# Kernel optimization log

Measured on AMD Instinct MI355X. Metric: run time of the kernel, lower is better.

## Reference

```python
import jax, jax.numpy as jnp
import numpy as np

N, IN_C, OUT_C, H = 100000, 256, 64, 8
K_CURV = 1.0      # manifold curvature k (Lorentz: t = sqrt(||s||^2 + k))
POWER_K = 2.0     # power_k of fp feature map


def fp(x, p):
    # norm(x) / (norm(x**p) + eps) * x**p, norms over last dim
    eps = 1e-12
    xp = x ** p
    norm_x = jnp.linalg.norm(x, axis=-1, keepdims=True)
    norm_xp = jnp.linalg.norm(xp, axis=-1, keepdims=True)
    return norm_x / (norm_xp + eps) * xp


def setup_inputs() -> dict:
    key = jax.random.key(0)
    ks = jax.random.split(key, 8)
    s = 1.0 / np.sqrt(IN_C)
    sm = 1.0 / np.sqrt(OUT_C)
    return {
        "query_input": jax.random.normal(ks[0], (N, IN_C), jnp.float32),
        # per-head HypLinear weights (stacked over heads)
        "Wq": jax.random.uniform(ks[1], (H, IN_C, OUT_C), jnp.float32, -s, s),
        "bq": jnp.zeros((H, OUT_C), jnp.float32),
        "Wk": jax.random.uniform(ks[2], (H, IN_C, OUT_C), jnp.float32, -s, s),
        "bk": jnp.zeros((H, OUT_C), jnp.float32),
        "Wv": jax.random.uniform(ks[3], (H, IN_C, OUT_C), jnp.float32, -s, s),
        "bv": jnp.zeros((H, OUT_C), jnp.float32),
        "norm_scale": jnp.ones((), jnp.float32),
        # v_map_mlp: Linear(out_channels, out_channels)
        "Wm": jax.random.uniform(ks[4], (OUT_C, OUT_C), jnp.float32, -sm, sm),
        "bm": jnp.zeros((OUT_C,), jnp.float32),
    }


def reference(query_input, Wq, bq, Wk, bk, Wv, bv, norm_scale, Wm, bm):
    # HypLinear per head: space part = x @ W + b; the time part
    # sqrt(||space||^2 + k) is dropped by [..., 1:] in linear_focus_attention,
    # so only the space components are computed.  shapes: [N, H, OUT_C]
    qs = jnp.einsum('nd,hdo->nho', query_input, Wq) + bq
    ks_ = jnp.einsum('nd,hdo->nho', query_input, Wk) + bk
    v = jnp.einsum('nd,hdo->nho', query_input, Wv) + bv

    denom_s = jnp.abs(norm_scale) + 1e-6
    phi_q = fp((jax.nn.relu(qs) + 1e-6) / denom_s, POWER_K)
    phi_k = fp((jax.nn.relu(ks_) + 1e-6) / denom_s, POWER_K)

    # linear attention: O(N * H * m * d)
    kT_v = jnp.einsum('nhm,nhd->hmd', phi_k, v)          # [H, m, d]
    numerator = jnp.einsum('nhm,hmd->nhd', phi_q, kT_v)  # [N, H, d]
    sum_k = phi_k.sum(axis=0)                            # [H, m]
    denominator = jnp.einsum('nhd,hd->nh', phi_q, sum_k)[..., None]
    attn = numerator / (denominator + 1e-6)

    # residual v-map MLP
    attn = attn + (jnp.einsum('nhd,de->nhe', v, Wm) + bm)

    # trans_heads_concat=False -> mean over heads
    out = attn.mean(axis=1)                              # [N, OUT_C]

    # lift back to Lorentz: prepend time component
    t = jnp.sqrt((out ** 2).sum(axis=-1, keepdims=True) + K_CURV)
    return jnp.concatenate([t, out], axis=-1)            # [N, OUT_C+1]
```

## Files before the change

kernel.cpp:

```cpp
#include <hip/hip_runtime.h>
#include <hip/hip_bf16.h>

#define NROWS 100000
#define NH 8
#define RPC 1568
#define NSUB 49
#define K2CH 98

typedef short s16x8 __attribute__((ext_vector_type(8)));
typedef float f32x4 __attribute__((ext_vector_type(4)));
typedef unsigned short u16;

__device__ __forceinline__ u16 f2bf(float f) {
  union { float f; unsigned u; } x; x.f = f;
  unsigned r = (x.u + 0x7FFFu + ((x.u >> 16) & 1u)) >> 16;
  return (u16)r;
}
__device__ __forceinline__ float bf2f(u16 b) {
  union { unsigned u; float f; } x; x.u = ((unsigned)b) << 16;
  return x.f;
}

__global__ __launch_bounds__(256) void k0_pack(
    const float* __restrict__ Wq, const float* __restrict__ Wk,
    const float* __restrict__ Wv, u16* __restrict__ Wp)
{
  int t = blockIdx.x * 256 + threadIdx.x;
  int lane = t & 63;
  int rest = t >> 6;
  int s = rest % 48;
  int hc = rest / 48;
  int c2 = hc & 1, h = hc >> 1;
  int ml = lane & 15, sgk = lane >> 4;
  const float* W; int col, ks;
  if (s < 32) { int tl = s >> 3; ks = s & 7; W = c2 ? Wk : Wq; col = tl * 16 + ml; }
  else        { int tv = (s >> 3) - 4; ks = s & 7; W = Wv; col = c2 * 32 + tv * 16 + ml; }
  int k0 = ks * 32 + sgk * 8;
  u16 o[8];
#pragma unroll
  for (int j = 0; j < 8; j++)
    o[j] = f2bf(W[((size_t)h * 256 + k0 + j) * 64 + col]);
  ushort4* dst = (ushort4*)(Wp + (size_t)t * 8);
  dst[0] = make_ushort4(o[0], o[1], o[2], o[3]);
  dst[1] = make_ushort4(o[4], o[5], o[6], o[7]);
}

__global__ __launch_bounds__(256, 2) void k1_gemm_phi(
    const float* __restrict__ x, const u16* __restrict__ Wp,
    const float* __restrict__ bq, const float* __restrict__ bk,
    const float* __restrict__ bv, const float* __restrict__ nsc,
    u16* __restrict__ phi_q, u16* __restrict__ phi_k, u16* __restrict__ vout)
{
  __shared__ u16 xs[32 * 256];
  __shared__ u16 vws[32 * 64 * 8];
  __shared__ u16 stq[4 * 16 * 72];
  __shared__ u16 stv[32 * 72];
  __shared__ float biasl[192];

  const int tid = threadIdx.x;
  const int wv = tid >> 6, lane = tid & 63;
  const int c2 = wv & 1, rg = wv >> 1;
  const int m = lane & 15, sg = lane >> 4;
  const int rc = blockIdx.x & 63, h = blockIdx.x >> 6;
  const int n0 = rc * RPC;

  if (tid < 192) {
    const float* bp = tid < 64 ? bq : (tid < 128 ? bk : bv);
    biasl[tid] = bp[h * 64 + (tid & 63)];
  }

  const u16* wb = Wp + (size_t)(h * 2 + c2) * (48 * 64 * 8);
  s16x8 wq[4][8];
#pragma unroll
  for (int t = 0; t < 4; t++)
#pragma unroll
    for (int ks = 0; ks < 8; ks++)
      wq[t][ks] = *(const s16x8*)(wb + ((t * 8 + ks) * 64 + lane) * 8);

#pragma unroll
  for (int i2 = 0; i2 < 8; i2++) {
    int u = tid + i2 * 256;
    int tl = u >> 9, ks = (u >> 6) & 7, ln = u & 63;
    const u16* src = Wp + ((size_t)(h * 2 + (tl >> 1)) * 48 + 32 + (tl & 1) * 8 + ks) * (64 * 8)
                     + (size_t)ln * 8;
    *(s16x8*)(vws + (size_t)u * 8) = *(const s16x8*)src;
  }

#pragma unroll
  for (int i = 0; i < 4; i++) {
    int cu = tid + i * 256;
    int row = cu >> 5, c = cu & 31;
    int n = n0 + row; if (n >= NROWS) n = NROWS - 1;
    const float* src = x + (size_t)n * 256 + c * 8;
    float4 f0 = *(const float4*)src;
    float4 f1 = *(const float4*)(src + 4);
    s16x8 pk;
    pk[0] = (short)f2bf(f0.x); pk[1] = (short)f2bf(f0.y);
    pk[2] = (short)f2bf(f0.z); pk[3] = (short)f2bf(f0.w);
    pk[4] = (short)f2bf(f1.x); pk[5] = (short)f2bf(f1.y);
    pk[6] = (short)f2bf(f1.z); pk[7] = (short)f2bf(f1.w);
    *(s16x8*)(xs + row * 256 + ((c ^ (row & 7)) * 8)) = pk;
  }
  __syncthreads();

  const float inv_denom = 1.0f / (fabsf(nsc[0]) + 1e-6f);
  u16* const xbase = xs + (rg * 16 + m) * 256;
  const int sw = m & 7;

  for (int s = 0; s < NSUB; s++) {
    float4 xl[8];
    if (s + 1 < NSUB) {
      int nb = n0 + (s + 1) * 32;
#pragma unroll
      for (int i = 0; i < 4; i++) {
        int cu = tid + i * 256;
        int row = cu >> 5, c = cu & 31;
        int n = nb + row; if (n >= NROWS) n = NROWS - 1;
        const float* src = x + (size_t)n * 256 + c * 8;
        xl[i * 2]     = *(const float4*)src;
        xl[i * 2 + 1] = *(const float4*)(src + 4);
      }
    }

    f32x4 aq[4], av[2];
#pragma unroll
    for (int t = 0; t < 4; t++) aq[t] = (f32x4){0.f, 0.f, 0.f, 0.f};
    av[0] = (f32x4){0.f, 0.f, 0.f, 0.f};
    av[1] = (f32x4){0.f, 0.f, 0.f, 0.f};
#pragma unroll
    for (int ks = 0; ks < 8; ks++) {
      s16x8 bf = *(const s16x8*)(xbase + (((ks * 4 + sg) ^ sw) * 8));
#pragma unroll
      for (int t = 0; t < 4; t++)
        aq[t] = __builtin_amdgcn_mfma_f32_16x16x32_bf16(wq[t][ks], bf, aq[t], 0, 0, 0);
      s16x8 vw0 = *(const s16x8*)(vws + (((c2 * 2 + 0) * 8 + ks) * 64 + lane) * 8);
      s16x8 vw1 = *(const s16x8*)(vws + (((c2 * 2 + 1) * 8 + ks) * 64 + lane) * 8);
      av[0] = __builtin_amdgcn_mfma_f32_16x16x32_bf16(vw0, bf, av[0], 0, 0, 0);
      av[1] = __builtin_amdgcn_mfma_f32_16x16x32_bf16(vw1, bf, av[1], 0, 0, 0);
    }

    f32x4 bqk[4], bvv[2];
#pragma unroll
    for (int t = 0; t < 4; t++) bqk[t] = *(const f32x4*)&biasl[c2 * 64 + t * 16 + sg * 4];
#pragma unroll
    for (int tv = 0; tv < 2; tv++) bvv[tv] = *(const f32x4*)&biasl[128 + c2 * 32 + tv * 16 + sg * 4];

    float vq[4][4];
    float s2 = 0.f, s4 = 0.f;
#pragma unroll
    for (int t = 0; t < 4; t++)
#pragma unroll
      for (int r = 0; r < 4; r++) {
        float y = (fmaxf(aq[t][r] + bqk[t][r], 0.f) + 1e-6f) * inv_denom;
        float y2 = y * y;
        vq[t][r] = y2;
        s2 += y2; s4 += y2 * y2;
      }
    s2 += __shfl_xor(s2, 16); s2 += __shfl_xor(s2, 32);
    s4 += __shfl_xor(s4, 16); s4 += __shfl_xor(s4, 32);
    float sc = sqrtf(s2) / (sqrtf(s4) + 1e-12f);

    {
      u16* sq = stq + wv * 1152 + m * 72;
#pragma unroll
      for (int t = 0; t < 4; t++)
        *(ushort4*)(sq + ((t + m) & 3) * 16 + sg * 4) =
          make_ushort4(f2bf(vq[t][0] * sc), f2bf(vq[t][1] * sc),
                       f2bf(vq[t][2] * sc), f2bf(vq[t][3] * sc));
      int rowl = rg * 16 + m;
      u16* sv = stv + rowl * 72;
#pragma unroll
      for (int tv = 0; tv < 2; tv++) {
        int tc = c2 * 2 + tv;
        f32x4 a = av[tv], b = bvv[tv];
        *(ushort4*)(sv + ((tc + rowl) & 3) * 16 + sg * 4) =
          make_ushort4(f2bf(a[0] + b[0]), f2bf(a[1] + b[1]),
                       f2bf(a[2] + b[2]), f2bf(a[3] + b[3]));
      }
    }
    {
      int r_ = lane >> 2, tc = lane & 3;
      const u16* a = stq + wv * 1152 + r_ * 72 + ((tc + r_) & 3) * 16;
      s16x8 p0 = *(const s16x8*)a;
      s16x8 p1 = *(const s16x8*)(a + 8);
      int n = n0 + s * 32 + rg * 16 + r_;
      if (n < NROWS) {
        u16* dst = (c2 ? phi_k : phi_q) + ((size_t)h * NROWS + n) * 64 + tc * 16;
        *(s16x8*)dst = p0;
        *(s16x8*)(dst + 8) = p1;
      }
    }
    __syncthreads();

    {
      int row = wv * 8 + (lane >> 3);
      int hc8 = lane & 7, tc = hc8 >> 1, half = hc8 & 1;
      const u16* a = stv + row * 72 + ((tc + row) & 3) * 16 + half * 8;
      s16x8 pv = *(const s16x8*)a;
      int n = n0 + s * 32 + row;
      if (n < NROWS)
        *(s16x8*)(vout + ((size_t)h * NROWS + n) * 64 + tc * 16 + half * 8) = pv;
    }
    if (s + 1 < NSUB) {
#pragma unroll
      for (int i = 0; i < 4; i++) {
        int cu = tid + i * 256;
        int row = cu >> 5, c = cu & 31;
        float4 f0 = xl[i * 2], f1 = xl[i * 2 + 1];
        s16x8 pk;
        pk[0] = (short)f2bf(f0.x); pk[1] = (short)f2bf(f0.y);
        pk[2] = (short)f2bf(f0.z); pk[3] = (short)f2bf(f0.w);
        pk[4] = (short)f2bf(f1.x); pk[5] = (short)f2bf(f1.y);
        pk[6] = (short)f2bf(f1.z); pk[7] = (short)f2bf(f1.w);
        *(s16x8*)(xs + row * 256 + ((c ^ (row & 7)) * 8)) = pk;
      }
    }
    __syncthreads();
  }
}

__global__ __launch_bounds__(256) void k2_ktv(
    const u16* __restrict__ phi_k, const u16* __restrict__ vin,
    float* __restrict__ P)
{
  __shared__ u16 pkT[2][64][72];
  __shared__ u16 vT[2][64][72];
  const int tid = threadIdx.x;
  const int h = blockIdx.y;
  const int r0 = blockIdx.x * 1024;
  const int wv = tid >> 6, lane = tid & 63;
  const int m = lane & 15, sg = lane >> 4;
  const int c4 = (tid & 15) * 4, rgp = tid >> 4;

  const u16* pkb = phi_k + (size_t)h * (NROWS * 64);
  const u16* vb  = vin  + (size_t)h * (NROWS * 64);

  f32x4 acc[4];
#pragma unroll
  for (int t = 0; t < 4; t++) acc[t] = (f32x4){0.f, 0.f, 0.f, 0.f};
  f32x4 accs = (f32x4){0.f, 0.f, 0.f, 0.f};
  s16x8 onesf;
#pragma unroll
  for (int j = 0; j < 8; j++) onesf[j] = (m == 0) ? (short)0x3F80 : (short)0;

  ushort4 pk4[4], vv4[4];
#define K2_LOAD(sub)                                                        \
  {                                                                         \
    int nb = r0 + (sub) * 64 + rgp * 4;                                     \
    _Pragma("unroll")                                                       \
    for (int i = 0; i < 4; i++) {                                           \
      int n = nb + i;                                                       \
      if (n < NROWS) {                                                      \
        pk4[i] = *(const ushort4*)(pkb + (size_t)n * 64 + c4);              \
        vv4[i] = *(const ushort4*)(vb  + (size_t)n * 64 + c4);              \
      } else {                                                              \
        pk4[i] = make_ushort4(0, 0, 0, 0);                                  \
        vv4[i] = make_ushort4(0, 0, 0, 0);                                  \
      }                                                                     \
    }                                                                       \
  }
#define K2_WRITE(buf)                                                       \
  {                                                                         \
    *(ushort4*)&pkT[buf][c4 + 0][rgp * 4] = make_ushort4(pk4[0].x, pk4[1].x, pk4[2].x, pk4[3].x); \
    *(ushort4*)&pkT[buf][c4 + 1][rgp * 4] = make_ushort4(pk4[0].y, pk4[1].y, pk4[2].y, pk4[3].y); \
    *(ushort4*)&pkT[buf][c4 + 2][rgp * 4] = make_ushort4(pk4[0].z, pk4[1].z, pk4[2].z, pk4[3].z); \
    *(ushort4*)&pkT[buf][c4 + 3][rgp * 4] = make_ushort4(pk4[0].w, pk4[1].w, pk4[2].w, pk4[3].w); \
    *(ushort4*)&vT[buf][c4 + 0][rgp * 4]  = make_ushort4(vv4[0].x, vv4[1].x, vv4[2].x, vv4[3].x); \
    *(ushort4*)&vT[buf][c4 + 1][rgp * 4]  = make_ushort4(vv4[0].y, vv4[1].y, vv4[2].y, vv4[3].y); \
    *(ushort4*)&vT[buf][c4 + 2][rgp * 4]  = make_ushort4(vv4[0].z, vv4[1].z, vv4[2].z, vv4[3].z); \
    *(ushort4*)&vT[buf][c4 + 3][rgp * 4]  = make_ushort4(vv4[0].w, vv4[1].w, vv4[2].w, vv4[3].w); \
  }

  K2_LOAD(0); K2_WRITE(0);
  __syncthreads();

  for (int sub = 0; sub < 16; sub++) {
    int cur = sub & 1;
    if (sub + 1 < 16) K2_LOAD(sub + 1);
#pragma unroll
    for (int ks = 0; ks < 2; ks++) {
      s16x8 af = *(const s16x8*)&pkT[cur][wv * 16 + m][ks * 32 + sg * 8];
#pragma unroll
      for (int t = 0; t < 4; t++) {
        s16x8 bfv = *(const s16x8*)&vT[cur][t * 16 + m][ks * 32 + sg * 8];
        acc[t] = __builtin_amdgcn_mfma_f32_16x16x32_bf16(af, bfv, acc[t], 0, 0, 0);
      }
      accs = __builtin_amdgcn_mfma_f32_16x16x32_bf16(af, onesf, accs, 0, 0, 0);
    }
    if (sub + 1 < 16) K2_WRITE(cur ^ 1);
    __syncthreads();
  }

  float* pb = P + (size_t)(blockIdx.x * NH + h) * (65 * 64);
  int mm = wv * 16 + sg * 4;
#pragma unroll
  for (int t = 0; t < 4; t++)
#pragma unroll
    for (int r = 0; r < 4; r++)
      pb[(t * 16 + m) * 64 + mm + r] = acc[t][r];
  if (m == 0)
#pragma unroll
    for (int r = 0; r < 4; r++)
      pb[64 * 64 + mm + r] = accs[r];
}

__global__ __launch_bounds__(256) void k25_pack(
    const float* __restrict__ P, const float* __restrict__ Wm,
    u16* __restrict__ kTvT, u16* __restrict__ WmP)
{
  int idx = blockIdx.x * 256 + threadIdx.x;
  if (idx < NH * 65 * 64) {
    float s = 0.f;
    for (int rcc = 0; rcc < K2CH; rcc++)
      s += P[(size_t)rcc * (NH * 65 * 64) + idx];
    kTvT[idx] = f2bf(s);
  } else if (idx < NH * 65 * 64 + 64 * 64) {
    int j = idx - NH * 65 * 64;
    WmP[j] = f2bf(Wm[(j & 63) * 64 + (j >> 6)]);
  }
}

__global__ __launch_bounds__(256) void k3_out(
    const u16* __restrict__ phi_q, const u16* __restrict__ vin,
    const u16* __restrict__ kTvT, const u16* __restrict__ WmP,
    const float* __restrict__ bm, float* __restrict__ out)
{
  const int tid = threadIdx.x;
  const int wv = tid >> 6, lane = tid & 63;
  const int m = lane & 15, sg = lane >> 4;
  const int n0 = blockIdx.x * 64;
  const int rw = wv * 16;
  const int n = n0 + rw + m;

  float bmv[4];
#pragma unroll
  for (int t = 0; t < 4; t++) bmv[t] = bm[t * 16 + m];

  s16x8 vbf[2];
#pragma unroll
  for (int ks = 0; ks < 2; ks++) {
    float a[8];
#pragma unroll
    for (int j = 0; j < 8; j++) a[j] = 0.f;
#pragma unroll
    for (int h = 0; h < NH; h++) {
      s16x8 v8 = *(const s16x8*)(vin + (size_t)h * (NROWS * 64) + (size_t)n * 64
                                 + ks * 32 + sg * 8);
#pragma unroll
      for (int j = 0; j < 8; j++) a[j] += bf2f((u16)v8[j]);
    }
#pragma unroll
    for (int j = 0; j < 8; j++) vbf[ks][j] = (short)f2bf(a[j] * 0.125f);
  }

  f32x4 zero4 = {0.f, 0.f, 0.f, 0.f};
  s16x8 zero8 = {0, 0, 0, 0, 0, 0, 0, 0};
  f32x4 osum[4];
#pragma unroll
  for (int t = 0; t < 4; t++) osum[t] = zero4;

  for (int h = 0; h < NH; h++) {
    const u16* pqb = phi_q + (size_t)h * (NROWS * 64) + (size_t)n * 64;
    const u16* kb = kTvT + (size_t)h * (65 * 64);
    f32x4 accn[4];
#pragma unroll
    for (int t = 0; t < 4; t++) accn[t] = zero4;
    f32x4 accd = zero4;
#pragma unroll
    for (int ks = 0; ks < 2; ks++) {
      s16x8 aq = *(const s16x8*)(pqb + ks * 32 + sg * 8);
#pragma unroll
      for (int t = 0; t < 4; t++) {
        s16x8 bfv = *(const s16x8*)(kb + (size_t)(t * 16 + m) * 64 + ks * 32 + sg * 8);
        accn[t] = __builtin_amdgcn_mfma_f32_16x16x32_bf16(aq, bfv, accn[t], 0, 0, 0);
      }
      s16x8 bd = zero8;
      if (m == 0)
        bd = *(const s16x8*)(kb + (size_t)64 * 64 + ks * 32 + sg * 8);
      accd = __builtin_amdgcn_mfma_f32_16x16x32_bf16(aq, bd, accd, 0, 0, 0);
    }
#pragma unroll
    for (int r = 0; r < 4; r++) {
      float den = __shfl(accd[r], lane & 48);
      float rinv = 1.0f / (den + 1e-6f);
#pragma unroll
      for (int t = 0; t < 4; t++) osum[t][r] += accn[t][r] * rinv;
    }
  }

  f32x4 accr[4];
#pragma unroll
  for (int t = 0; t < 4; t++) accr[t] = zero4;
#pragma unroll
  for (int ks = 0; ks < 2; ks++)
#pragma unroll
    for (int t = 0; t < 4; t++) {
      s16x8 bw = *(const s16x8*)(WmP + (size_t)(t * 16 + m) * 64 + ks * 32 + sg * 8);
      accr[t] = __builtin_amdgcn_mfma_f32_16x16x32_bf16(vbf[ks], bw, accr[t], 0, 0, 0);
    }

#pragma unroll
  for (int r = 0; r < 4; r++) {
    int nn = n0 + rw + sg * 4 + r;
    float v4[4];
    float ssq = 0.f;
#pragma unroll
    for (int t = 0; t < 4; t++) {
      float o = osum[t][r] * 0.125f + accr[t][r] + bmv[t];
      v4[t] = o;
      ssq += o * o;
    }
    ssq += __shfl_xor(ssq, 1);
    ssq += __shfl_xor(ssq, 2);
    ssq += __shfl_xor(ssq, 4);
    ssq += __shfl_xor(ssq, 8);
    if (nn < NROWS) {
      if (m == 0) out[(size_t)nn * 65] = sqrtf(ssq + 1.0f);
#pragma unroll
      for (int t = 0; t < 4; t++)
        out[(size_t)nn * 65 + 1 + t * 16 + m] = v4[t];
    }
  }
}

extern "C" void kernel_launch(void* const* d_in, const int* in_sizes, int n_in,
                              void* d_out, int out_size, void* d_ws, size_t ws_size,
                              hipStream_t stream) {
  const float* x   = (const float*)d_in[0];
  const float* Wq  = (const float*)d_in[1];
  const float* bq  = (const float*)d_in[2];
  const float* Wk  = (const float*)d_in[3];
  const float* bk  = (const float*)d_in[4];
  const float* Wv  = (const float*)d_in[5];
  const float* bv  = (const float*)d_in[6];
  const float* nsc = (const float*)d_in[7];
  const float* Wm  = (const float*)d_in[8];
  const float* bm  = (const float*)d_in[9];
  float* out = (float*)d_out;

  char* ws = (char*)d_ws;
  const size_t PHI_BYTES = (size_t)NROWS * NH * 64 * 2;
  u16* phi_q = (u16*)(ws);
  u16* phi_k = (u16*)(ws + PHI_BYTES);
  u16* vv    = (u16*)(ws + 2 * PHI_BYTES);
  u16* Wp    = (u16*)(ws + 3 * PHI_BYTES);
  char* p    = ws + 3 * PHI_BYTES + 786432;
  float* P   = (float*)(p);
  u16* kTvT  = (u16*)(p + 13066240);
  u16* WmP   = (u16*)(p + 13066240 + 66560);

  k0_pack<<<192, 256, 0, stream>>>(Wq, Wk, Wv, Wp);
  k1_gemm_phi<<<512, 256, 0, stream>>>(x, Wp, bq, bk, bv, nsc, phi_q, phi_k, vv);
  dim3 g2(K2CH, NH);
  k2_ktv<<<g2, 256, 0, stream>>>(phi_k, vv, P);
  k25_pack<<<(NH * 65 * 64 + 64 * 64 + 255) / 256, 256, 0, stream>>>(P, Wm, kTvT, WmP);
  k3_out<<<(NROWS + 63) / 64, 256, 0, stream>>>(phi_q, vv, kTvT, WmP, bm, out);
}
```

Baseline: 449.0 us.

## Fuse kᵀv reduction into projection kernel and fold V-map into precomputed weight

The projection kernel now accumulates phi_kᵀ·v and the phi_k column sums per block with MFMA, so phi_k and v are never written to global memory and the separate k2 pass is removed. The residual v-map MLP is folded algebraically into a precomputed 256x64 weight (mean of Wv over heads times Wm), which k3 applies directly to bf16 x. A separate pre-pass converts x to bf16 once, replacing the in-kernel LDS staging. The cost is an extra conversion kernel, unstaged global reads of x in k1, and a larger GEMM in k3.

```diff
diff --git a/kernel.cpp b/kernel.cpp
--- a/kernel.cpp
+++ b/kernel.cpp
@@ -5,7 +5,7 @@
 #define NH 8
 #define RPC 1568
 #define NSUB 49
-#define K2CH 98
+#define NCH 64
 
 typedef short s16x8 __attribute__((ext_vector_type(8)));
 typedef float f32x4 __attribute__((ext_vector_type(4)));
@@ -19,6 +19,17 @@
 __device__ __forceinline__ float bf2f(u16 b) {
   union { unsigned u; float f; } x; x.u = ((unsigned)b) << 16;
   return x.f;
+}
+
+__global__ __launch_bounds__(256) void k_cvt(
+    const float* __restrict__ x, u16* __restrict__ xb)
+{
+  size_t idx = (size_t)(blockIdx.x * 256 + threadIdx.x) * 8;
+  if (idx >= (size_t)NROWS * 256) return;
+  float4 f0 = *(const float4*)(x + idx);
+  float4 f1 = *(const float4*)(x + idx + 4);
+  *(ushort4*)(xb + idx)     = make_ushort4(f2bf(f0.x), f2bf(f0.y), f2bf(f0.z), f2bf(f0.w));
+  *(ushort4*)(xb + idx + 4) = make_ushort4(f2bf(f1.x), f2bf(f1.y), f2bf(f1.z), f2bf(f1.w));
 }
 
 __global__ __launch_bounds__(256) void k0_pack(
@@ -45,16 +56,54 @@
   dst[1] = make_ushort4(o[4], o[5], o[6], o[7]);
 }
 
+__global__ __launch_bounds__(256) void kW(
+    const float* __restrict__ Wv, const float* __restrict__ bv,
+    const float* __restrict__ Wm, const float* __restrict__ bm,
+    u16* __restrict__ WrP, float* __restrict__ br)
+{
+  __shared__ float wvb[4][64];
+  int tid = threadIdx.x;
+  int b = blockIdx.x;
+  {
+    int kl = tid >> 6, d = tid & 63;
+    float s = 0.f;
+#pragma unroll
+    for (int h = 0; h < NH; h++)
+      s += Wv[((size_t)h * 256 + b * 4 + kl) * 64 + d];
+    wvb[kl][d] = s * 0.125f;
+  }
+  __syncthreads();
+  {
+    int kl = tid >> 6, e = tid & 63;
+    float acc = 0.f;
+#pragma unroll
+    for (int d = 0; d < 64; d++)
+      acc += wvb[kl][d] * Wm[d * 64 + e];
+    WrP[e * 256 + b * 4 + kl] = f2bf(acc);
+  }
+  if (b == 0 && tid < 64) {
+    int e = tid;
+    float s = 0.f;
+    for (int d = 0; d < 64; d++) {
+      float vb = 0.f;
+#pragma unroll
+      for (int h = 0; h < NH; h++) vb += bv[h * 64 + d];
+      s += 0.125f * vb * Wm[d * 64 + e];
+    }
+    br[e] = s + bm[e];
+  }
+}
+
 __global__ __launch_bounds__(256, 2) void k1_gemm_phi(
-    const float* __restrict__ x, const u16* __restrict__ Wp,
+    const u16* __restrict__ xb, const u16* __restrict__ Wp,
     const float* __restrict__ bq, const float* __restrict__ bk,
     const float* __restrict__ bv, const float* __restrict__ nsc,
-    u16* __restrict__ phi_q, u16* __restrict__ phi_k, u16* __restrict__ vout)
-{
-  __shared__ u16 xs[32 * 256];
-  __shared__ u16 vws[32 * 64 * 8];
-  __shared__ u16 stq[4 * 16 * 72];
-  __shared__ u16 stv[32 * 72];
+    u16* __restrict__ phi_q, float* __restrict__ P)
+{
+  __shared__ u16 vws[2048 * 8];
+  __shared__ u16 pkT[64][36];
+  __shared__ u16 vT[64][36];
+  __shared__ u16 stq[2][16][72];
   __shared__ float biasl[192];
 
   const int tid = threadIdx.x;
@@ -85,42 +134,23 @@
                      + (size_t)ln * 8;
     *(s16x8*)(vws + (size_t)u * 8) = *(const s16x8*)src;
   }
-
-#pragma unroll
-  for (int i = 0; i < 4; i++) {
-    int cu = tid + i * 256;
-    int row = cu >> 5, c = cu & 31;
-    int n = n0 + row; if (n >= NROWS) n = NROWS - 1;
-    const float* src = x + (size_t)n * 256 + c * 8;
-    float4 f0 = *(const float4*)src;
-    float4 f1 = *(const float4*)(src + 4);
-    s16x8 pk;
-    pk[0] = (short)f2bf(f0.x); pk[1] = (short)f2bf(f0.y);
-    pk[2] = (short)f2bf(f0.z); pk[3] = (short)f2bf(f0.w);
-    pk[4] = (short)f2bf(f1.x); pk[5] = (short)f2bf(f1.y);
-    pk[6] = (short)f2bf(f1.z); pk[7] = (short)f2bf(f1.w);
-    *(s16x8*)(xs + row * 256 + ((c ^ (row & 7)) * 8)) = pk;
-  }
   __syncthreads();
 
   const float inv_denom = 1.0f / (fabsf(nsc[0]) + 1e-6f);
-  u16* const xbase = xs + (rg * 16 + m) * 256;
-  const int sw = m & 7;
+  const int rowl = rg * 16 + m;
+
+  f32x4 kacc[4];
+#pragma unroll
+  for (int t = 0; t < 4; t++) kacc[t] = (f32x4){0.f, 0.f, 0.f, 0.f};
+  f32x4 sacc = (f32x4){0.f, 0.f, 0.f, 0.f};
+  s16x8 onesf;
+#pragma unroll
+  for (int j = 0; j < 8; j++) onesf[j] = (m == 0) ? (short)0x3F80 : (short)0;
 
   for (int s = 0; s < NSUB; s++) {
-    float4 xl[8];
-    if (s + 1 < NSUB) {
-      int nb = n0 + (s + 1) * 32;
-#pragma unroll
-      for (int i = 0; i < 4; i++) {
-        int cu = tid + i * 256;
-        int row = cu >> 5, c = cu & 31;
-        int n = nb + row; if (n >= NROWS) n = NROWS - 1;
-        const float* src = x + (size_t)n * 256 + c * 8;
-        xl[i * 2]     = *(const float4*)src;
-        xl[i * 2 + 1] = *(const float4*)(src + 4);
-      }
-    }
+    int nrow = n0 + s * 32 + rowl;
+    bool valid = nrow < NROWS;
+    const u16* xrow = xb + (size_t)(valid ? nrow : NROWS - 1) * 256;
 
     f32x4 aq[4], av[2];
 #pragma unroll
@@ -129,7 +159,7 @@
     av[1] = (f32x4){0.f, 0.f, 0.f, 0.f};
 #pragma unroll
     for (int ks = 0; ks < 8; ks++) {
-      s16x8 bf = *(const s16x8*)(xbase + (((ks * 4 + sg) ^ sw) * 8));
+      s16x8 bf = *(const s16x8*)(xrow + ks * 32 + sg * 8);
 #pragma unroll
       for (int t = 0; t < 4; t++)
         aq[t] = __builtin_amdgcn_mfma_f32_16x16x32_bf16(wq[t][ks], bf, aq[t], 0, 0, 0);
@@ -159,171 +189,81 @@
     s2 += __shfl_xor(s2, 16); s2 += __shfl_xor(s2, 32);
     s4 += __shfl_xor(s4, 16); s4 += __shfl_xor(s4, 32);
     float sc = sqrtf(s2) / (sqrtf(s4) + 1e-12f);
-
-    {
-      u16* sq = stq + wv * 1152 + m * 72;
+    float scm = valid ? sc : 0.f;
+
+    if (c2 == 0) {
+      u16* sq = &stq[rg][0][0] + m * 72;
 #pragma unroll
       for (int t = 0; t < 4; t++)
         *(ushort4*)(sq + ((t + m) & 3) * 16 + sg * 4) =
           make_ushort4(f2bf(vq[t][0] * sc), f2bf(vq[t][1] * sc),
                        f2bf(vq[t][2] * sc), f2bf(vq[t][3] * sc));
-      int rowl = rg * 16 + m;
-      u16* sv = stv + rowl * 72;
-#pragma unroll
-      for (int tv = 0; tv < 2; tv++) {
-        int tc = c2 * 2 + tv;
-        f32x4 a = av[tv], b = bvv[tv];
-        *(ushort4*)(sv + ((tc + rowl) & 3) * 16 + sg * 4) =
-          make_ushort4(f2bf(a[0] + b[0]), f2bf(a[1] + b[1]),
-                       f2bf(a[2] + b[2]), f2bf(a[3] + b[3]));
-      }
-    }
-    {
       int r_ = lane >> 2, tc = lane & 3;
-      const u16* a = stq + wv * 1152 + r_ * 72 + ((tc + r_) & 3) * 16;
+      const u16* a = &stq[rg][0][0] + r_ * 72 + ((tc + r_) & 3) * 16;
       s16x8 p0 = *(const s16x8*)a;
       s16x8 p1 = *(const s16x8*)(a + 8);
       int n = n0 + s * 32 + rg * 16 + r_;
       if (n < NROWS) {
-        u16* dst = (c2 ? phi_k : phi_q) + ((size_t)h * NROWS + n) * 64 + tc * 16;
+        u16* dst = phi_q + ((size_t)h * NROWS + n) * 64 + tc * 16;
         *(s16x8*)dst = p0;
         *(s16x8*)(dst + 8) = p1;
       }
-    }
+    } else {
+#pragma unroll
+      for (int t = 0; t < 4; t++)
+#pragma unroll
+        for (int r = 0; r < 4; r++)
+          pkT[t * 16 + sg * 4 + r][rowl] = f2bf(vq[t][r] * scm);
+    }
+#pragma unroll
+    for (int tv = 0; tv < 2; tv++)
+#pragma unroll
+      for (int r = 0; r < 4; r++) {
+        float vval = valid ? (av[tv][r] + bvv[tv][r]) : 0.f;
+        vT[c2 * 32 + tv * 16 + sg * 4 + r][rowl] = f2bf(vval);
+      }
     __syncthreads();
 
     {
-      int row = wv * 8 + (lane >> 3);
-      int hc8 = lane & 7, tc = hc8 >> 1, half = hc8 & 1;
-      const u16* a = stv + row * 72 + ((tc + row) & 3) * 16 + half * 8;
-      s16x8 pv = *(const s16x8*)a;
-      int n = n0 + s * 32 + row;
-      if (n < NROWS)
-        *(s16x8*)(vout + ((size_t)h * NROWS + n) * 64 + tc * 16 + half * 8) = pv;
-    }
-    if (s + 1 < NSUB) {
-#pragma unroll
-      for (int i = 0; i < 4; i++) {
-        int cu = tid + i * 256;
-        int row = cu >> 5, c = cu & 31;
-        float4 f0 = xl[i * 2], f1 = xl[i * 2 + 1];
-        s16x8 pk;
-        pk[0] = (short)f2bf(f0.x); pk[1] = (short)f2bf(f0.y);
-        pk[2] = (short)f2bf(f0.z); pk[3] = (short)f2bf(f0.w);
-        pk[4] = (short)f2bf(f1.x); pk[5] = (short)f2bf(f1.y);
-        pk[6] = (short)f2bf(f1.z); pk[7] = (short)f2bf(f1.w);
-        *(s16x8*)(xs + row * 256 + ((c ^ (row & 7)) * 8)) = pk;
-      }
+      s16x8 afr = *(const s16x8*)&pkT[wv * 16 + m][sg * 8];
+#pragma unroll
+      for (int t = 0; t < 4; t++) {
+        s16x8 bfr = *(const s16x8*)&vT[t * 16 + m][sg * 8];
+        kacc[t] = __builtin_amdgcn_mfma_f32_16x16x32_bf16(afr, bfr, kacc[t], 0, 0, 0);
+      }
+      sacc = __builtin_amdgcn_mfma_f32_16x16x32_bf16(afr, onesf, sacc, 0, 0, 0);
     }
     __syncthreads();
   }
-}
-
-__global__ __launch_bounds__(256) void k2_ktv(
-    const u16* __restrict__ phi_k, const u16* __restrict__ vin,
-    float* __restrict__ P)
-{
-  __shared__ u16 pkT[2][64][72];
-  __shared__ u16 vT[2][64][72];
-  const int tid = threadIdx.x;
-  const int h = blockIdx.y;
-  const int r0 = blockIdx.x * 1024;
-  const int wv = tid >> 6, lane = tid & 63;
-  const int m = lane & 15, sg = lane >> 4;
-  const int c4 = (tid & 15) * 4, rgp = tid >> 4;
-
-  const u16* pkb = phi_k + (size_t)h * (NROWS * 64);
-  const u16* vb  = vin  + (size_t)h * (NROWS * 64);
-
-  f32x4 acc[4];
-#pragma unroll
-  for (int t = 0; t < 4; t++) acc[t] = (f32x4){0.f, 0.f, 0.f, 0.f};
-  f32x4 accs = (f32x4){0.f, 0.f, 0.f, 0.f};
-  s16x8 onesf;
-#pragma unroll
-  for (int j = 0; j < 8; j++) onesf[j] = (m == 0) ? (short)0x3F80 : (short)0;
-
-  ushort4 pk4[4], vv4[4];
-#define K2_LOAD(sub)                                                        \
-  {                                                                         \
-    int nb = r0 + (sub) * 64 + rgp * 4;                                     \
-    _Pragma("unroll")                                                       \
-    for (int i = 0; i < 4; i++) {                                           \
-      int n = nb + i;                                                       \
-      if (n < NROWS) {                                                      \
-        pk4[i] = *(const ushort4*)(pkb + (size_t)n * 64 + c4);              \
-        vv4[i] = *(const ushort4*)(vb  + (size_t)n * 64 + c4);              \
-      } else {                                                              \
-        pk4[i] = make_ushort4(0, 0, 0, 0);                                  \
-        vv4[i] = make_ushort4(0, 0, 0, 0);                                  \
-      }                                                                     \
-    }                                                                       \
-  }
-#define K2_WRITE(buf)                                                       \
-  {                                                                         \
-    *(ushort4*)&pkT[buf][c4 + 0][rgp * 4] = make_ushort4(pk4[0].x, pk4[1].x, pk4[2].x, pk4[3].x); \
-    *(ushort4*)&pkT[buf][c4 + 1][rgp * 4] = make_ushort4(pk4[0].y, pk4[1].y, pk4[2].y, pk4[3].y); \
-    *(ushort4*)&pkT[buf][c4 + 2][rgp * 4] = make_ushort4(pk4[0].z, pk4[1].z, pk4[2].z, pk4[3].z); \
-    *(ushort4*)&pkT[buf][c4 + 3][rgp * 4] = make_ushort4(pk4[0].w, pk4[1].w, pk4[2].w, pk4[3].w); \
-    *(ushort4*)&vT[buf][c4 + 0][rgp * 4]  = make_ushort4(vv4[0].x, vv4[1].x, vv4[2].x, vv4[3].x); \
-    *(ushort4*)&vT[buf][c4 + 1][rgp * 4]  = make_ushort4(vv4[0].y, vv4[1].y, vv4[2].y, vv4[3].y); \
-    *(ushort4*)&vT[buf][c4 + 2][rgp * 4]  = make_ushort4(vv4[0].z, vv4[1].z, vv4[2].z, vv4[3].z); \
-    *(ushort4*)&vT[buf][c4 + 3][rgp * 4]  = make_ushort4(vv4[0].w, vv4[1].w, vv4[2].w, vv4[3].w); \
-  }
-
-  K2_LOAD(0); K2_WRITE(0);
-  __syncthreads();
-
-  for (int sub = 0; sub < 16; sub++) {
-    int cur = sub & 1;
-    if (sub + 1 < 16) K2_LOAD(sub + 1);
-#pragma unroll
-    for (int ks = 0; ks < 2; ks++) {
-      s16x8 af = *(const s16x8*)&pkT[cur][wv * 16 + m][ks * 32 + sg * 8];
-#pragma unroll
-      for (int t = 0; t < 4; t++) {
-        s16x8 bfv = *(const s16x8*)&vT[cur][t * 16 + m][ks * 32 + sg * 8];
-        acc[t] = __builtin_amdgcn_mfma_f32_16x16x32_bf16(af, bfv, acc[t], 0, 0, 0);
-      }
-      accs = __builtin_amdgcn_mfma_f32_16x16x32_bf16(af, onesf, accs, 0, 0, 0);
-    }
-    if (sub + 1 < 16) K2_WRITE(cur ^ 1);
-    __syncthreads();
-  }
-
-  float* pb = P + (size_t)(blockIdx.x * NH + h) * (65 * 64);
-  int mm = wv * 16 + sg * 4;
+
+  float* pb = P + (size_t)blockIdx.x * 4160;
 #pragma unroll
   for (int t = 0; t < 4; t++)
 #pragma unroll
     for (int r = 0; r < 4; r++)
-      pb[(t * 16 + m) * 64 + mm + r] = acc[t][r];
+      pb[(t * 16 + m) * 64 + wv * 16 + sg * 4 + r] = kacc[t][r];
   if (m == 0)
 #pragma unroll
     for (int r = 0; r < 4; r++)
-      pb[64 * 64 + mm + r] = accs[r];
-}
-
-__global__ __launch_bounds__(256) void k25_pack(
-    const float* __restrict__ P, const float* __restrict__ Wm,
-    u16* __restrict__ kTvT, u16* __restrict__ WmP)
+      pb[4096 + wv * 16 + sg * 4 + r] = sacc[r];
+}
+
+__global__ __launch_bounds__(256) void k25_reduce(
+    const float* __restrict__ P, u16* __restrict__ kTvT)
 {
   int idx = blockIdx.x * 256 + threadIdx.x;
-  if (idx < NH * 65 * 64) {
-    float s = 0.f;
-    for (int rcc = 0; rcc < K2CH; rcc++)
-      s += P[(size_t)rcc * (NH * 65 * 64) + idx];
-    kTvT[idx] = f2bf(s);
-  } else if (idx < NH * 65 * 64 + 64 * 64) {
-    int j = idx - NH * 65 * 64;
-    WmP[j] = f2bf(Wm[(j & 63) * 64 + (j >> 6)]);
-  }
+  if (idx >= NH * 4160) return;
+  int h = idx / 4160, i = idx - h * 4160;
+  float s = 0.f;
+  for (int rcc = 0; rcc < NCH; rcc++)
+    s += P[(size_t)(rcc + 64 * h) * 4160 + i];
+  kTvT[idx] = f2bf(s);
 }
 
 __global__ __launch_bounds__(256) void k3_out(
-    const u16* __restrict__ phi_q, const u16* __restrict__ vin,
-    const u16* __restrict__ kTvT, const u16* __restrict__ WmP,
-    const float* __restrict__ bm, float* __restrict__ out)
+    const u16* __restrict__ phi_q, const u16* __restrict__ xb,
+    const u16* __restrict__ kTvT, const u16* __restrict__ WrP,
+    const float* __restrict__ br, float* __restrict__ out)
 {
   const int tid = threadIdx.x;
   const int wv = tid >> 6, lane = tid & 63;
@@ -331,27 +271,11 @@
   const int n0 = blockIdx.x * 64;
   const int rw = wv * 16;
   const int n = n0 + rw + m;
-
-  float bmv[4];
-#pragma unroll
-  for (int t = 0; t < 4; t++) bmv[t] = bm[t * 16 + m];
-
-  s16x8 vbf[2];
-#pragma unroll
-  for (int ks = 0; ks < 2; ks++) {
-    float a[8];
-#pragma unroll
-    for (int j = 0; j < 8; j++) a[j] = 0.f;
-#pragma unroll
-    for (int h = 0; h < NH; h++) {
-      s16x8 v8 = *(const s16x8*)(vin + (size_t)h * (NROWS * 64) + (size_t)n * 64
-                                 + ks * 32 + sg * 8);
-#pragma unroll
-      for (int j = 0; j < 8; j++) a[j] += bf2f((u16)v8[j]);
-    }
-#pragma unroll
-    for (int j = 0; j < 8; j++) vbf[ks][j] = (short)f2bf(a[j] * 0.125f);
-  }
+  const int nc = n < NROWS ? n : NROWS - 1;
+
+  float brv[4];
+#pragma unroll
+  for (int t = 0; t < 4; t++) brv[t] = br[t * 16 + m];
 
   f32x4 zero4 = {0.f, 0.f, 0.f, 0.f};
   s16x8 zero8 = {0, 0, 0, 0, 0, 0, 0, 0};
@@ -360,8 +284,8 @@
   for (int t = 0; t < 4; t++) osum[t] = zero4;
 
   for (int h = 0; h < NH; h++) {
-    const u16* pqb = phi_q + (size_t)h * (NROWS * 64) + (size_t)n * 64;
-    const u16* kb = kTvT + (size_t)h * (65 * 64);
+    const u16* pqb = phi_q + ((size_t)h * NROWS + nc) * 64;
+    const u16* kb = kTvT + h * 4160;
     f32x4 accn[4];
 #pragma unroll
     for (int t = 0; t < 4; t++) accn[t] = zero4;
@@ -376,7 +300,7 @@
       }
       s16x8 bd = zero8;
       if (m == 0)
-        bd = *(const s16x8*)(kb + (size_t)64 * 64 + ks * 32 + sg * 8);
+        bd = *(const s16x8*)(kb + 4096 + ks * 32 + sg * 8);
       accd = __builtin_amdgcn_mfma_f32_16x16x32_bf16(aq, bd, accd, 0, 0, 0);
     }
 #pragma unroll
@@ -391,13 +315,16 @@
   f32x4 accr[4];
 #pragma unroll
   for (int t = 0; t < 4; t++) accr[t] = zero4;
-#pragma unroll
-  for (int ks = 0; ks < 2; ks++)
+  const u16* xrow = xb + (size_t)nc * 256;
+#pragma unroll
+  for (int ks = 0; ks < 8; ks++) {
+    s16x8 ax = *(const s16x8*)(xrow + ks * 32 + sg * 8);
 #pragma unroll
     for (int t = 0; t < 4; t++) {
-      s16x8 bw = *(const s16x8*)(WmP + (size_t)(t * 16 + m) * 64 + ks * 32 + sg * 8);
-      accr[t] = __builtin_amdgcn_mfma_f32_16x16x32_bf16(vbf[ks], bw, accr[t], 0, 0, 0);
-    }
+      s16x8 bw = *(const s16x8*)(WrP + (size_t)(t * 16 + m) * 256 + ks * 32 + sg * 8);
+      accr[t] = __builtin_amdgcn_mfma_f32_16x16x32_bf16(ax, bw, accr[t], 0, 0, 0);
+    }
+  }
 
 #pragma unroll
   for (int r = 0; r < 4; r++) {
@@ -406,7 +333,7 @@
     float ssq = 0.f;
 #pragma unroll
     for (int t = 0; t < 4; t++) {
-      float o = osum[t][r] * 0.125f + accr[t][r] + bmv[t];
+      float o = osum[t][r] * 0.125f + accr[t][r] + brv[t];
       v4[t] = o;
       ssq += o * o;
     }
@@ -439,20 +366,18 @@
   float* out = (float*)d_out;
 
   char* ws = (char*)d_ws;
-  const size_t PHI_BYTES = (size_t)NROWS * NH * 64 * 2;
-  u16* phi_q = (u16*)(ws);
-  u16* phi_k = (u16*)(ws + PHI_BYTES);
-  u16* vv    = (u16*)(ws + 2 * PHI_BYTES);
-  u16* Wp    = (u16*)(ws + 3 * PHI_BYTES);
-  char* p    = ws + 3 * PHI_BYTES + 786432;
-  float* P   = (float*)(p);
-  u16* kTvT  = (u16*)(p + 13066240);
-  u16* WmP   = (u16*)(p + 13066240 + 66560);
-
+  u16* xb    = (u16*)(ws);
+  u16* phi_q = (u16*)(ws + 51200000);
+  u16* Wp    = (u16*)(ws + 153600000);
+  float* P   = (float*)(ws + 154386432);
+  u16* kTvT  = (u16*)(ws + 162906112);
+  u16* WrP   = (u16*)(ws + 162972672);
+  float* br  = (float*)(ws + 163005440);
+
+  k_cvt<<<12500, 256, 0, stream>>>(x, xb);
   k0_pack<<<192, 256, 0, stream>>>(Wq, Wk, Wv, Wp);
-  k1_gemm_phi<<<512, 256, 0, stream>>>(x, Wp, bq, bk, bv, nsc, phi_q, phi_k, vv);
-  dim3 g2(K2CH, NH);
-  k2_ktv<<<g2, 256, 0, stream>>>(phi_k, vv, P);
-  k25_pack<<<(NH * 65 * 64 + 64 * 64 + 255) / 256, 256, 0, stream>>>(P, Wm, kTvT, WmP);
-  k3_out<<<(NROWS + 63) / 64, 256, 0, stream>>>(phi_q, vv, kTvT, WmP, bm, out);
-}
+  kW<<<64, 256, 0, stream>>>(Wv, bv, Wm, bm, WrP, br);
+  k1_gemm_phi<<<512, 256, 0, stream>>>(xb, Wp, bq, bk, bv, nsc, phi_q, P);
+  k25_reduce<<<130, 256, 0, stream>>>(P, kTvT);
+  k3_out<<<1563, 256, 0, stream>>>(phi_q, xb, kTvT, WrP, br, out);
+}
```

Measured after the change: 451.6 us. No clear change (+0.6%).
